# Optimization experiments

Measured on AMD Instinct MI355X. Metric: run time of the kernel, lower is better.

## Reference

```python
import jax, jax.numpy as jnp
import numpy as np

NMS_THRESH = 0.5
SCORE_THRESH = 0.2
MAX_SUBJECT = 15
MAX_OBJECT = 15
B, NS, NO = 32, 512, 512


def _make_boxes(k, b, n):
    u = jax.random.uniform(k, (b, n, 4))
    xy = u[..., :2] * 1000.0          # top-left corner
    wh = u[..., 2:] * 200.0 + 1.0     # positive width/height
    return jnp.concatenate([xy, xy + wh], axis=-1)  # valid xyxy boxes


def setup_inputs() -> dict:
    key = jax.random.key(0)
    ks = jax.random.split(key, 6)
    return {
        "subj_boxes": _make_boxes(ks[0], B, NS),
        "subj_scores": jax.random.uniform(ks[1], (B, NS)),
        "subj_labels": jax.random.randint(ks[2], (B, NS), 0, 30, dtype=jnp.int32),
        "obj_boxes": _make_boxes(ks[3], B, NO),
        "obj_scores": jax.random.uniform(ks[4], (B, NO)),
        "obj_labels": jax.random.randint(ks[5], (B, NO), 0, 30, dtype=jnp.int32),
    }


def reference(subj_boxes, subj_scores, subj_labels, obj_boxes, obj_scores, obj_labels):
    # concat subject + object detections per image, as in preprocess()
    boxes = jnp.concatenate([subj_boxes, obj_boxes], axis=1)    # [B,N,4]
    scores = jnp.concatenate([subj_scores, obj_scores], axis=1) # [B,N]
    labels = jnp.concatenate([subj_labels, obj_labels], axis=1) # [B,N]
    b, n = scores.shape
    is_subj = jnp.arange(n) < subj_boxes.shape[1]               # [N]

    # sort by score descending (matches the argsort after NMS; greedy NMS
    # preserves this ordering among survivors)
    order = jnp.argsort(-scores, axis=1)
    boxes = jnp.take_along_axis(boxes, order[..., None], axis=1)
    scores = jnp.take_along_axis(scores, order, axis=1)
    labels = jnp.take_along_axis(labels, order, axis=1)
    is_subj = jnp.take(is_subj, order)                          # [B,N]

    active = scores >= SCORE_THRESH

    # torchvision batched_nms: offset boxes per class so distinct classes
    # never overlap (comparisons only -> no gradient path)
    max_coord = jax.lax.stop_gradient(jnp.max(boxes))
    ob = boxes + labels.astype(boxes.dtype)[..., None] * (max_coord + 1.0)

    # pairwise IoU [B,N,N]
    area = (ob[..., 2] - ob[..., 0]) * (ob[..., 3] - ob[..., 1])
    lt = jnp.maximum(ob[:, :, None, :2], ob[:, None, :, :2])
    rb = jnp.minimum(ob[:, :, None, 2:], ob[:, None, :, 2:])
    wh = jnp.clip(rb - lt, 0.0)
    inter = wh[..., 0] * wh[..., 1]
    iou = inter / (area[:, :, None] + area[:, None, :] - inter)

    later = jnp.arange(n)[None, :] > jnp.arange(n)[:, None]     # strictly lower-score

    def body(i, suppressed):  # greedy NMS, vectorized over batch
        keep_i = active[:, i] & ~suppressed[:, i]
        return suppressed | (keep_i[:, None] & (iou[:, i, :] > NMS_THRESH) & later[i])

    suppressed = jax.lax.fori_loop(0, n, body, jnp.zeros((b, n), dtype=bool))
    kept = active & ~suppressed

    # split survivors into subjects / objects, keep top max_subject/max_object
    neg = jnp.finfo(scores.dtype).min
    sub_key = jnp.where(kept & is_subj, scores, neg)
    obj_key = jnp.where(kept & ~is_subj, scores, neg)
    sv, si = jax.lax.top_k(sub_key, MAX_SUBJECT)
    ov, oi = jax.lax.top_k(obj_key, MAX_OBJECT)
    idx = jnp.concatenate([si, oi], axis=1)                     # [B,K]
    valid = jnp.concatenate([sv, ov], axis=1) > neg             # [B,K]

    out_boxes = jnp.take_along_axis(boxes, idx[..., None], axis=1) * valid[..., None]
    out_scores = jnp.take_along_axis(scores, idx, axis=1) * valid
    out_labels = jnp.where(valid, jnp.take_along_axis(labels, idx, axis=1), -1)
    num_subjects = jnp.sum(sv > neg, axis=1)
    return out_boxes, out_scores, out_labels, num_subjects, valid
```

## Files before the change

### kernel.cpp

```cpp
#include <hip/hip_runtime.h>
#include <stdint.h>

#define BQ    32
#define NSUB  512
#define NDET  1024
#define NCLS  30
#define KSLOT 30
#define BCAP  96

#pragma clang fp contract(off)

typedef unsigned long long u64;

__global__ __launch_bounds__(512) void bucket_kernel(
    const float* __restrict__ sb, const float* __restrict__ ss,
    const int*   __restrict__ sl,
    const float* __restrict__ ob, const float* __restrict__ os,
    const int*   __restrict__ ol,
    float* __restrict__ pmax, int* __restrict__ cnts,
    u64* __restrict__ bkeys, float4* __restrict__ bboxes)
{
    const int b = blockIdx.x, t = threadIdx.x;
    const int lane = t & 63, w = t >> 6;
    __shared__ int   lcnt[NCLS];
    __shared__ float wred[8];

    if (t < NCLS) lcnt[t] = 0;

    float4 bxs = *(const float4*)(sb + (size_t)(b * NSUB + t) * 4);
    float4 bxo = *(const float4*)(ob + (size_t)(b * NSUB + t) * 4);
    float scs = ss[b * NSUB + t];  int lbs = sl[b * NSUB + t];
    float sco = os[b * NSUB + t];  int lbo = ol[b * NSUB + t];

    float m = fmaxf(fmaxf(fmaxf(bxs.x, bxs.y), fmaxf(bxs.z, bxs.w)),
                    fmaxf(fmaxf(bxo.x, bxo.y), fmaxf(bxo.z, bxo.w)));
    for (int off = 32; off; off >>= 1) m = fmaxf(m, __shfl_xor(m, off));
    if (lane == 0) wred[w] = m;
    __syncthreads();
    if (t == 0) {
        float mm = wred[0];
        for (int i = 1; i < 8; ++i) mm = fmaxf(mm, wred[i]);
        pmax[b] = mm;
    }

    if (scs >= 0.2f) {
        int pos = atomicAdd(&lcnt[lbs], 1);
        if (pos < BCAP) {
            size_t s = ((size_t)b * NCLS + lbs) * BCAP + pos;
            bkeys[s]  = ((u64)__float_as_uint(scs) << 32) | (u64)(1023 - t);
            bboxes[s] = bxs;
        }
    }
    if (sco >= 0.2f) {
        int pos = atomicAdd(&lcnt[lbo], 1);
        if (pos < BCAP) {
            size_t s = ((size_t)b * NCLS + lbo) * BCAP + pos;
            bkeys[s]  = ((u64)__float_as_uint(sco) << 32) | (u64)(1023 - (512 + t));
            bboxes[s] = bxo;
        }
    }
    __syncthreads();
    if (t < NCLS) {
        int c = lcnt[t];
        cnts[b * NCLS + t] = (c < BCAP) ? c : BCAP;
    }
}

__global__ __launch_bounds__(64) void nms_class_kernel(
    const float* __restrict__ pmax, const int* __restrict__ cnts,
    const u64* __restrict__ bkeys, const float4* __restrict__ bboxes,
    u64* __restrict__ subk, u64* __restrict__ objk)
{
#pragma clang fp contract(off)
    const int c    = blockIdx.x;
    const int b    = blockIdx.y;
    const int lane = threadIdx.x;

    __shared__ u64    keyarr[BCAP];
    __shared__ u64    skey[BCAP];
    __shared__ float4 bxs4[BCAP];

    const size_t base = (size_t)b * NCLS + c;

    u64    K1 = bkeys[base * BCAP + lane];
    float4 B1 = bboxes[base * BCAP + lane];
    u64 K2 = 0; float4 B2 = make_float4(0.f, 0.f, 0.f, 0.f);
    if (lane < BCAP - 64) {
        K2 = bkeys[base * BCAP + 64 + lane];
        B2 = bboxes[base * BCAP + 64 + lane];
    }
    const int cnt = cnts[base];
    float pv = pmax[lane & 31];
    for (int off = 32; off; off >>= 1) pv = fmaxf(pv, __shfl_xor(pv, off));
    const float mco  = pv + 1.0f;
    const float offc = (float)c * mco;

    keyarr[lane] = K1;
    if (lane < BCAP - 64) keyarr[64 + lane] = K2;
    __threadfence_block();

    {
        int r = 0;
        for (int l = 0; l < cnt; ++l) r += (keyarr[l] > K1) ? 1 : 0;
        if (lane < cnt) { skey[r] = K1; bxs4[r] = B1; }
    }
    if (cnt > 64) {
        int e = 64 + lane;
        int r = 0;
        for (int l = 0; l < cnt; ++l) r += (keyarr[l] > K2) ? 1 : 0;
        if (e < cnt) { skey[r] = K2; bxs4[r] = B2; }
    }
    __threadfence_block();

    const int  lim1  = (cnt < 64) ? cnt : 64;
    const bool have1 = (lane < lim1);
    u64 SK1 = have1 ? skey[lane] : 0;
    int idx1 = 1023 - (int)(unsigned)(SK1 & 0xffffffffull);
    float4 bj1 = have1 ? bxs4[lane] : make_float4(0.f, 0.f, 0.f, 0.f);
    const bool have2 = (64 + lane) < cnt;
    u64 SK2 = 0; int idx2 = 0; float4 bj2 = make_float4(0.f, 0.f, 0.f, 0.f);
    if (cnt > 64) {
        SK2 = have2 ? skey[64 + lane] : 0;
        idx2 = 1023 - (int)(unsigned)(SK2 & 0xffffffffull);
        if (have2) bj2 = bxs4[64 + lane];
    }

    float j0 = bj1.x + offc, j1 = bj1.y + offc;
    float j2v = bj1.z + offc, j3 = bj1.w + offc;
    float aj = (j2v - j0) * (j3 - j1);
    u64 ov = 0;
    for (int l = 0; l < lim1; ++l) {
        float4 bl = bxs4[l];
        float i0 = bl.x + offc, i1 = bl.y + offc;
        float i2 = bl.z + offc, i3 = bl.w + offc;
        float ai = (i2 - i0) * (i3 - i1);
        if (have1 && l < lane) {
            float ltx = fmaxf(i0, j0), lty = fmaxf(i1, j1);
            float rbx = fminf(i2, j2v), rby = fminf(i3, j3);
            float wx = fmaxf(rbx - ltx, 0.0f), wy = fmaxf(rby - lty, 0.0f);
            float inter = wx * wy;
            float iou = inter / ((ai + aj) - inter);
            if (iou > 0.5f) ov |= (1ull << l);
        }
    }
    bool sup1 = !have1;
    for (int l = 0; l < lim1; ++l) {
        u64 bal = __ballot(sup1);
        if (!((bal >> l) & 1ull)) sup1 = sup1 || (((ov >> l) & 1ull) != 0ull);
    }
    const bool kept1 = have1 && !sup1;
    const u64 keptA = __ballot(kept1);

    bool kept2 = false;
    if (cnt > 64) {
        float k0 = bj2.x + offc, k1 = bj2.y + offc;
        float k2 = bj2.z + offc, k3 = bj2.w + offc;
        float ak = (k2 - k0) * (k3 - k1);
        bool sup2 = !have2;
        for (int l = 0; l < 64; ++l) {
            if ((keptA >> l) & 1ull) {
                float4 bl = bxs4[l];
                float i0 = bl.x + offc, i1 = bl.y + offc;
                float i2 = bl.z + offc, i3 = bl.w + offc;
                float ai = (i2 - i0) * (i3 - i1);
                if (!sup2) {
                    float ltx = fmaxf(i0, k0), lty = fmaxf(i1, k1);
                    float rbx = fminf(i2, k2), rby = fminf(i3, k3);
                    float wx = fmaxf(rbx - ltx, 0.0f), wy = fmaxf(rby - lty, 0.0f);
                    float inter = wx * wy;
                    float iou = inter / ((ai + ak) - inter);
                    if (iou > 0.5f) sup2 = true;
                }
            }
        }
        u64 ov2 = 0;
        const int lim2 = cnt - 64;
        for (int l = 0; l < lim2; ++l) {
            float4 bl = bxs4[64 + l];
            float i0 = bl.x + offc, i1 = bl.y + offc;
            float i2 = bl.z + offc, i3 = bl.w + offc;
            float ai = (i2 - i0) * (i3 - i1);
            if (have2 && l < lane) {
                float ltx = fmaxf(i0, k0), lty = fmaxf(i1, k1);
                float rbx = fminf(i2, k2), rby = fminf(i3, k3);
                float wx = fmaxf(rbx - ltx, 0.0f), wy = fmaxf(rby - lty, 0.0f);
                float inter = wx * wy;
                float iou = inter / ((ai + ak) - inter);
                if (iou > 0.5f) ov2 |= (1ull << l);
            }
        }
        for (int l = 0; l < lim2; ++l) {
            u64 bal = __ballot(sup2);
            if (!((bal >> l) & 1ull)) sup2 = sup2 || (((ov2 >> l) & 1ull) != 0ull);
        }
        kept2 = have2 && !sup2;
    }

    const bool s1 = kept1 && (idx1 < NSUB), o1 = kept1 && (idx1 >= NSUB);
    const bool s2 = kept2 && (idx2 < NSUB), o2 = kept2 && (idx2 >= NSUB);
    const u64 mS1 = __ballot(s1), mS2 = __ballot(s2);
    const u64 mO1 = __ballot(o1), mO2 = __ballot(o2);
    const u64 ltm = (1ull << lane) - 1ull;
    u64* subp = subk + base * 15;
    u64* objp = objk + base * 15;
    if (s1) { int p = (int)__popcll(mS1 & ltm); if (p < 15) subp[p] = SK1; }
    if (s2) { int p = (int)__popcll(mS1) + (int)__popcll(mS2 & ltm); if (p < 15) subp[p] = SK2; }
    if (o1) { int p = (int)__popcll(mO1 & ltm); if (p < 15) objp[p] = SK1; }
    if (o2) { int p = (int)__popcll(mO1) + (int)__popcll(mO2 & ltm); if (p < 15) objp[p] = SK2; }
    int tS = (int)(__popcll(mS1) + __popcll(mS2)); if (tS > 15) tS = 15;
    int tO = (int)(__popcll(mO1) + __popcll(mO2)); if (tO > 15) tO = 15;
    if (lane >= tS && lane < 15) subp[lane] = 0;
    if (lane >= tO && lane < 15) objp[lane] = 0;
}

__global__ __launch_bounds__(64) void select_kernel(
    const float* __restrict__ sb, const int* __restrict__ sl,
    const float* __restrict__ ob, const int* __restrict__ ol,
    const u64* __restrict__ subk, const u64* __restrict__ objk,
    float* __restrict__ out)
{
    const int b    = blockIdx.x;
    const int side = blockIdx.y;
    const int lane = threadIdx.x;

    float* outB = out;
    float* outS = out + BQ * KSLOT * 4;
    float* outL = outS + BQ * KSLOT;
    float* outN = outL + BQ * KSLOT;
    float* outV = outN + BQ;

    const u64* src = (side ? objk : subk) + (size_t)b * NCLS * 15;
    u64 kk[8];
    #pragma unroll
    for (int i = 0; i < 8; ++i) {
        int p = lane + 64 * i;
        kk[i] = (p < NCLS * 15) ? src[p] : 0;
    }
    int nvalid = 0;
    for (int r = 0; r < 15; ++r) {
        u64 lm = 0; int li = 0;
        #pragma unroll
        for (int i = 0; i < 8; ++i) if (kk[i] > lm) { lm = kk[i]; li = i; }
        u64 gm = lm;
        for (int off = 32; off; off >>= 1) {
            u64 o = __shfl_xor(gm, off);
            if (o > gm) gm = o;
        }
        int p = b * KSLOT + (side ? (15 + r) : r);
        if (gm == 0) {
            if (lane == 0) {
                *(float4*)(outB + (size_t)p * 4) = make_float4(0.f, 0.f, 0.f, 0.f);
                outS[p] = 0.0f; outL[p] = -1.0f; outV[p] = 0.0f;
            }
        } else {
            u64 win = __ballot(lm == gm);
            int wl = (int)__ffsll(win) - 1;
            if (lane == wl) {
                kk[li] = 0;
                int idx = 1023 - (int)(unsigned)(gm & 0xffffffffull);
                float score = __uint_as_float((unsigned)(gm >> 32));
                float4 bx; int lb;
                if (idx < NSUB) {
                    bx = *(const float4*)(sb + (size_t)(b * NSUB + idx) * 4);
                    lb = sl[b * NSUB + idx];
                } else {
                    bx = *(const float4*)(ob + (size_t)(b * NSUB + idx - NSUB) * 4);
                    lb = ol[b * NSUB + idx - NSUB];
                }
                *(float4*)(outB + (size_t)p * 4) = bx;
                outS[p] = score;
                outL[p] = (float)lb;
                outV[p] = 1.0f;
            }
            nvalid++;
        }
    }
    if (side == 0 && lane == 0) outN[b] = (float)nvalid;
}

extern "C" void kernel_launch(void* const* d_in, const int* in_sizes, int n_in,
                              void* d_out, int out_size, void* d_ws, size_t ws_size,
                              hipStream_t stream) {
    const float* sb = (const float*)d_in[0];
    const float* ss = (const float*)d_in[1];
    const int*   sl = (const int*)d_in[2];
    const float* ob = (const float*)d_in[3];
    const float* os = (const float*)d_in[4];
    const int*   ol = (const int*)d_in[5];

    float*  pmax   = (float*)d_ws;
    int*    cnts   = (int*)((char*)d_ws + 256);
    u64*    bkeys  = (u64*)((char*)d_ws + 8192);
    float4* bboxes = (float4*)((char*)d_ws + 745472);
    u64*    subk   = (u64*)((char*)d_ws + 2220032);
    u64*    objk   = subk + (size_t)BQ * NCLS * 15;

    bucket_kernel<<<dim3(BQ), dim3(512), 0, stream>>>(
        sb, ss, sl, ob, os, ol, pmax, cnts, bkeys, bboxes);
    nms_class_kernel<<<dim3(NCLS, BQ), dim3(64), 0, stream>>>(
        pmax, cnts, bkeys, bboxes, subk, objk);
    select_kernel<<<dim3(BQ, 2), dim3(64), 0, stream>>>(
        sb, sl, ob, ol, subk, objk, (float*)d_out);
}
```

Measured before the change: 88.54 us.

## Fuse bucketing, per-class NMS and top-k selection into one per-image kernel

```diff
diff --git a/kernel.cpp b/kernel.cpp
--- a/kernel.cpp
+++ b/kernel.cpp
@@ -7,275 +7,259 @@
 #define NCLS  30
 #define KSLOT 30
 #define BCAP  96
+#define NTHR  1024
+#define NWAVE 16
 
 #pragma clang fp contract(off)
 
 typedef unsigned long long u64;
 
-__global__ __launch_bounds__(512) void bucket_kernel(
+__global__ __launch_bounds__(NTHR, 1) void fused_nms_kernel(
     const float* __restrict__ sb, const float* __restrict__ ss,
     const int*   __restrict__ sl,
     const float* __restrict__ ob, const float* __restrict__ os,
     const int*   __restrict__ ol,
-    float* __restrict__ pmax, int* __restrict__ cnts,
-    u64* __restrict__ bkeys, float4* __restrict__ bboxes)
+    float* __restrict__ out)
 {
+#pragma clang fp contract(off)
     const int b = blockIdx.x, t = threadIdx.x;
     const int lane = t & 63, w = t >> 6;
-    __shared__ int   lcnt[NCLS];
-    __shared__ float wred[8];
-
-    if (t < NCLS) lcnt[t] = 0;
-
-    float4 bxs = *(const float4*)(sb + (size_t)(b * NSUB + t) * 4);
-    float4 bxo = *(const float4*)(ob + (size_t)(b * NSUB + t) * 4);
-    float scs = ss[b * NSUB + t];  int lbs = sl[b * NSUB + t];
-    float sco = os[b * NSUB + t];  int lbo = ol[b * NSUB + t];
-
-    float m = fmaxf(fmaxf(fmaxf(bxs.x, bxs.y), fmaxf(bxs.z, bxs.w)),
-                    fmaxf(fmaxf(bxo.x, bxo.y), fmaxf(bxo.z, bxo.w)));
+
+    __shared__ u64    bkey[NCLS][BCAP];
+    __shared__ float4 bbox[NCLS][BCAP];
+    __shared__ u64    skey[NWAVE][BCAP];
+    __shared__ float4 sbox[NWAVE][BCAP];
+    __shared__ u64    outk[2][NCLS * 15];
+    __shared__ float4 outbx[2][NCLS * 15];
+    __shared__ int    lcnt[NCLS];
+    __shared__ float  wred[NWAVE];
+    __shared__ float  gmaxs;
+
+    const float4* sb4 = (const float4*)sb;
+    const float4* ob4 = (const float4*)ob;
+
+    float m = -__builtin_inff();
+    for (int i = t; i < BQ * NSUB; i += NTHR) {
+        float4 a = sb4[i], c4 = ob4[i];
+        m = fmaxf(m, fmaxf(fmaxf(a.x, a.y), fmaxf(a.z, a.w)));
+        m = fmaxf(m, fmaxf(fmaxf(c4.x, c4.y), fmaxf(c4.z, c4.w)));
+    }
     for (int off = 32; off; off >>= 1) m = fmaxf(m, __shfl_xor(m, off));
     if (lane == 0) wred[w] = m;
+    if (t < NCLS) lcnt[t] = 0;
     __syncthreads();
     if (t == 0) {
         float mm = wred[0];
-        for (int i = 1; i < 8; ++i) mm = fmaxf(mm, wred[i]);
-        pmax[b] = mm;
-    }
-
-    if (scs >= 0.2f) {
-        int pos = atomicAdd(&lcnt[lbs], 1);
-        if (pos < BCAP) {
-            size_t s = ((size_t)b * NCLS + lbs) * BCAP + pos;
-            bkeys[s]  = ((u64)__float_as_uint(scs) << 32) | (u64)(1023 - t);
-            bboxes[s] = bxs;
-        }
-    }
-    if (sco >= 0.2f) {
-        int pos = atomicAdd(&lcnt[lbo], 1);
-        if (pos < BCAP) {
-            size_t s = ((size_t)b * NCLS + lbo) * BCAP + pos;
-            bkeys[s]  = ((u64)__float_as_uint(sco) << 32) | (u64)(1023 - (512 + t));
-            bboxes[s] = bxo;
+        for (int i = 1; i < NWAVE; ++i) mm = fmaxf(mm, wred[i]);
+        gmaxs = mm;
+    }
+
+    {
+        float4 bx; float sc; int lb;
+        if (t < NSUB) {
+            bx = sb4[b * NSUB + t];
+            sc = ss[b * NSUB + t];
+            lb = sl[b * NSUB + t];
+        } else {
+            int j = t - NSUB;
+            bx = ob4[b * NSUB + j];
+            sc = os[b * NSUB + j];
+            lb = ol[b * NSUB + j];
+        }
+        if (sc >= 0.2f) {
+            int pos = atomicAdd(&lcnt[lb], 1);
+            if (pos < BCAP) {
+                bkey[lb][pos] = ((u64)__float_as_uint(sc) << 32) | (u64)(1023 - t);
+                bbox[lb][pos] = bx;
+            }
         }
     }
     __syncthreads();
-    if (t < NCLS) {
-        int c = lcnt[t];
-        cnts[b * NCLS + t] = (c < BCAP) ? c : BCAP;
-    }
-}
-
-__global__ __launch_bounds__(64) void nms_class_kernel(
-    const float* __restrict__ pmax, const int* __restrict__ cnts,
-    const u64* __restrict__ bkeys, const float4* __restrict__ bboxes,
-    u64* __restrict__ subk, u64* __restrict__ objk)
-{
-#pragma clang fp contract(off)
-    const int c    = blockIdx.x;
-    const int b    = blockIdx.y;
-    const int lane = threadIdx.x;
-
-    __shared__ u64    keyarr[BCAP];
-    __shared__ u64    skey[BCAP];
-    __shared__ float4 bxs4[BCAP];
-
-    const size_t base = (size_t)b * NCLS + c;
-
-    u64    K1 = bkeys[base * BCAP + lane];
-    float4 B1 = bboxes[base * BCAP + lane];
-    u64 K2 = 0; float4 B2 = make_float4(0.f, 0.f, 0.f, 0.f);
-    if (lane < BCAP - 64) {
-        K2 = bkeys[base * BCAP + 64 + lane];
-        B2 = bboxes[base * BCAP + 64 + lane];
-    }
-    const int cnt = cnts[base];
-    float pv = pmax[lane & 31];
-    for (int off = 32; off; off >>= 1) pv = fmaxf(pv, __shfl_xor(pv, off));
-    const float mco  = pv + 1.0f;
-    const float offc = (float)c * mco;
-
-    keyarr[lane] = K1;
-    if (lane < BCAP - 64) keyarr[64 + lane] = K2;
-    __threadfence_block();
-
-    {
-        int r = 0;
-        for (int l = 0; l < cnt; ++l) r += (keyarr[l] > K1) ? 1 : 0;
-        if (lane < cnt) { skey[r] = K1; bxs4[r] = B1; }
-    }
-    if (cnt > 64) {
-        int e = 64 + lane;
-        int r = 0;
-        for (int l = 0; l < cnt; ++l) r += (keyarr[l] > K2) ? 1 : 0;
-        if (e < cnt) { skey[r] = K2; bxs4[r] = B2; }
-    }
-    __threadfence_block();
-
-    const int  lim1  = (cnt < 64) ? cnt : 64;
-    const bool have1 = (lane < lim1);
-    u64 SK1 = have1 ? skey[lane] : 0;
-    int idx1 = 1023 - (int)(unsigned)(SK1 & 0xffffffffull);
-    float4 bj1 = have1 ? bxs4[lane] : make_float4(0.f, 0.f, 0.f, 0.f);
-    const bool have2 = (64 + lane) < cnt;
-    u64 SK2 = 0; int idx2 = 0; float4 bj2 = make_float4(0.f, 0.f, 0.f, 0.f);
-    if (cnt > 64) {
-        SK2 = have2 ? skey[64 + lane] : 0;
-        idx2 = 1023 - (int)(unsigned)(SK2 & 0xffffffffull);
-        if (have2) bj2 = bxs4[64 + lane];
-    }
-
-    float j0 = bj1.x + offc, j1 = bj1.y + offc;
-    float j2v = bj1.z + offc, j3 = bj1.w + offc;
-    float aj = (j2v - j0) * (j3 - j1);
-    u64 ov = 0;
-    for (int l = 0; l < lim1; ++l) {
-        float4 bl = bxs4[l];
-        float i0 = bl.x + offc, i1 = bl.y + offc;
-        float i2 = bl.z + offc, i3 = bl.w + offc;
-        float ai = (i2 - i0) * (i3 - i1);
-        if (have1 && l < lane) {
-            float ltx = fmaxf(i0, j0), lty = fmaxf(i1, j1);
-            float rbx = fminf(i2, j2v), rby = fminf(i3, j3);
-            float wx = fmaxf(rbx - ltx, 0.0f), wy = fmaxf(rby - lty, 0.0f);
-            float inter = wx * wy;
-            float iou = inter / ((ai + aj) - inter);
-            if (iou > 0.5f) ov |= (1ull << l);
-        }
-    }
-    bool sup1 = !have1;
-    for (int l = 0; l < lim1; ++l) {
-        u64 bal = __ballot(sup1);
-        if (!((bal >> l) & 1ull)) sup1 = sup1 || (((ov >> l) & 1ull) != 0ull);
-    }
-    const bool kept1 = have1 && !sup1;
-    const u64 keptA = __ballot(kept1);
-
-    bool kept2 = false;
-    if (cnt > 64) {
-        float k0 = bj2.x + offc, k1 = bj2.y + offc;
-        float k2 = bj2.z + offc, k3 = bj2.w + offc;
-        float ak = (k2 - k0) * (k3 - k1);
-        bool sup2 = !have2;
-        for (int l = 0; l < 64; ++l) {
-            if ((keptA >> l) & 1ull) {
-                float4 bl = bxs4[l];
+    const float mco = gmaxs + 1.0f;
+
+    for (int rr = 0; rr < 2; ++rr) {
+        const int c = w + NWAVE * rr;
+        if (c >= NCLS) break;
+        int cnt = lcnt[c]; if (cnt > BCAP) cnt = BCAP;
+        const float offc = (float)c * mco;
+
+        u64    K1 = bkey[c][lane];
+        float4 B1 = bbox[c][lane];
+        u64 K2 = 0; float4 B2 = make_float4(0.f, 0.f, 0.f, 0.f);
+        if (lane < BCAP - 64) {
+            K2 = bkey[c][64 + lane];
+            B2 = bbox[c][64 + lane];
+        }
+
+        {
+            int r = 0;
+            for (int l = 0; l < cnt; ++l) r += (bkey[c][l] > K1) ? 1 : 0;
+            if (lane < cnt) { skey[w][r] = K1; sbox[w][r] = B1; }
+        }
+        if (cnt > 64) {
+            int e = 64 + lane;
+            int r = 0;
+            for (int l = 0; l < cnt; ++l) r += (bkey[c][l] > K2) ? 1 : 0;
+            if (e < cnt) { skey[w][r] = K2; sbox[w][r] = B2; }
+        }
+        __threadfence_block();
+
+        const int  lim1  = (cnt < 64) ? cnt : 64;
+        const bool have1 = (lane < lim1);
+        u64 SK1 = have1 ? skey[w][lane] : 0;
+        int idx1 = 1023 - (int)(unsigned)(SK1 & 0xffffffffull);
+        float4 bj1 = have1 ? sbox[w][lane] : make_float4(0.f, 0.f, 0.f, 0.f);
+        const bool have2 = (64 + lane) < cnt;
+        u64 SK2 = 0; int idx2 = 0; float4 bj2 = make_float4(0.f, 0.f, 0.f, 0.f);
+        if (cnt > 64) {
+            SK2 = have2 ? skey[w][64 + lane] : 0;
+            idx2 = 1023 - (int)(unsigned)(SK2 & 0xffffffffull);
+            if (have2) bj2 = sbox[w][64 + lane];
+        }
+
+        float j0 = bj1.x + offc, j1 = bj1.y + offc;
+        float j2v = bj1.z + offc, j3 = bj1.w + offc;
+        float aj = (j2v - j0) * (j3 - j1);
+        u64 ov = 0;
+        for (int l = 0; l < lim1; ++l) {
+            float4 bl = sbox[w][l];
+            float i0 = bl.x + offc, i1 = bl.y + offc;
+            float i2 = bl.z + offc, i3 = bl.w + offc;
+            float ai = (i2 - i0) * (i3 - i1);
+            if (have1 && l < lane) {
+                float ltx = fmaxf(i0, j0), lty = fmaxf(i1, j1);
+                float rbx = fminf(i2, j2v), rby = fminf(i3, j3);
+                float wx = fmaxf(rbx - ltx, 0.0f), wy = fmaxf(rby - lty, 0.0f);
+                float inter = wx * wy;
+                float iou = inter / ((ai + aj) - inter);
+                if (iou > 0.5f) ov |= (1ull << l);
+            }
+        }
+        bool sup1 = !have1;
+        for (int l = 0; l < lim1; ++l) {
+            u64 bal = __ballot(sup1);
+            if (!((bal >> l) & 1ull)) sup1 = sup1 || (((ov >> l) & 1ull) != 0ull);
+        }
+        const bool kept1 = have1 && !sup1;
+        const u64 keptA = __ballot(kept1);
+
+        bool kept2 = false;
+        if (cnt > 64) {
+            float k0 = bj2.x + offc, k1 = bj2.y + offc;
+            float k2 = bj2.z + offc, k3 = bj2.w + offc;
+            float ak = (k2 - k0) * (k3 - k1);
+            bool sup2 = !have2;
+            for (int l = 0; l < 64; ++l) {
+                if ((keptA >> l) & 1ull) {
+                    float4 bl = sbox[w][l];
+                    float i0 = bl.x + offc, i1 = bl.y + offc;
+                    float i2 = bl.z + offc, i3 = bl.w + offc;
+                    float ai = (i2 - i0) * (i3 - i1);
+                    if (!sup2) {
+                        float ltx = fmaxf(i0, k0), lty = fmaxf(i1, k1);
+                        float rbx = fminf(i2, k2), rby = fminf(i3, k3);
+                        float wx = fmaxf(rbx - ltx, 0.0f), wy = fmaxf(rby - lty, 0.0f);
+                        float inter = wx * wy;
+                        float iou = inter / ((ai + ak) - inter);
+                        if (iou > 0.5f) sup2 = true;
+                    }
+                }
+            }
+            u64 ov2 = 0;
+            const int lim2 = cnt - 64;
+            for (int l = 0; l < lim2; ++l) {
+                float4 bl = sbox[w][64 + l];
                 float i0 = bl.x + offc, i1 = bl.y + offc;
                 float i2 = bl.z + offc, i3 = bl.w + offc;
                 float ai = (i2 - i0) * (i3 - i1);
-                if (!sup2) {
+                if (have2 && l < lane) {
                     float ltx = fmaxf(i0, k0), lty = fmaxf(i1, k1);
                     float rbx = fminf(i2, k2), rby = fminf(i3, k3);
                     float wx = fmaxf(rbx - ltx, 0.0f), wy = fmaxf(rby - lty, 0.0f);
                     float inter = wx * wy;
                     float iou = inter / ((ai + ak) - inter);
-                    if (iou > 0.5f) sup2 = true;
-                }
-            }
-        }
-        u64 ov2 = 0;
-        const int lim2 = cnt - 64;
-        for (int l = 0; l < lim2; ++l) {
-            float4 bl = bxs4[64 + l];
-            float i0 = bl.x + offc, i1 = bl.y + offc;
-            float i2 = bl.z + offc, i3 = bl.w + offc;
-            float ai = (i2 - i0) * (i3 - i1);
-            if (have2 && l < lane) {
-                float ltx = fmaxf(i0, k0), lty = fmaxf(i1, k1);
-                float rbx = fminf(i2, k2), rby = fminf(i3, k3);
-                float wx = fmaxf(rbx - ltx, 0.0f), wy = fmaxf(rby - lty, 0.0f);
-                float inter = wx * wy;
-                float iou = inter / ((ai + ak) - inter);
-                if (iou > 0.5f) ov2 |= (1ull << l);
-            }
-        }
-        for (int l = 0; l < lim2; ++l) {
-            u64 bal = __ballot(sup2);
-            if (!((bal >> l) & 1ull)) sup2 = sup2 || (((ov2 >> l) & 1ull) != 0ull);
-        }
-        kept2 = have2 && !sup2;
-    }
-
-    const bool s1 = kept1 && (idx1 < NSUB), o1 = kept1 && (idx1 >= NSUB);
-    const bool s2 = kept2 && (idx2 < NSUB), o2 = kept2 && (idx2 >= NSUB);
-    const u64 mS1 = __ballot(s1), mS2 = __ballot(s2);
-    const u64 mO1 = __ballot(o1), mO2 = __ballot(o2);
-    const u64 ltm = (1ull << lane) - 1ull;
-    u64* subp = subk + base * 15;
-    u64* objp = objk + base * 15;
-    if (s1) { int p = (int)__popcll(mS1 & ltm); if (p < 15) subp[p] = SK1; }
-    if (s2) { int p = (int)__popcll(mS1) + (int)__popcll(mS2 & ltm); if (p < 15) subp[p] = SK2; }
-    if (o1) { int p = (int)__popcll(mO1 & ltm); if (p < 15) objp[p] = SK1; }
-    if (o2) { int p = (int)__popcll(mO1) + (int)__popcll(mO2 & ltm); if (p < 15) objp[p] = SK2; }
-    int tS = (int)(__popcll(mS1) + __popcll(mS2)); if (tS > 15) tS = 15;
-    int tO = (int)(__popcll(mO1) + __popcll(mO2)); if (tO > 15) tO = 15;
-    if (lane >= tS && lane < 15) subp[lane] = 0;
-    if (lane >= tO && lane < 15) objp[lane] = 0;
-}
-
-__global__ __launch_bounds__(64) void select_kernel(
-    const float* __restrict__ sb, const int* __restrict__ sl,
-    const float* __restrict__ ob, const int* __restrict__ ol,
-    const u64* __restrict__ subk, const u64* __restrict__ objk,
-    float* __restrict__ out)
-{
-    const int b    = blockIdx.x;
-    const int side = blockIdx.y;
-    const int lane = threadIdx.x;
-
-    float* outB = out;
-    float* outS = out + BQ * KSLOT * 4;
-    float* outL = outS + BQ * KSLOT;
-    float* outN = outL + BQ * KSLOT;
-    float* outV = outN + BQ;
-
-    const u64* src = (side ? objk : subk) + (size_t)b * NCLS * 15;
-    u64 kk[8];
-    #pragma unroll
-    for (int i = 0; i < 8; ++i) {
-        int p = lane + 64 * i;
-        kk[i] = (p < NCLS * 15) ? src[p] : 0;
-    }
-    int nvalid = 0;
-    for (int r = 0; r < 15; ++r) {
-        u64 lm = 0; int li = 0;
+                    if (iou > 0.5f) ov2 |= (1ull << l);
+                }
+            }
+            for (int l = 0; l < lim2; ++l) {
+                u64 bal = __ballot(sup2);
+                if (!((bal >> l) & 1ull)) sup2 = sup2 || (((ov2 >> l) & 1ull) != 0ull);
+            }
+            kept2 = have2 && !sup2;
+        }
+
+        const bool s1 = kept1 && (idx1 < NSUB), o1 = kept1 && (idx1 >= NSUB);
+        const bool s2 = kept2 && (idx2 < NSUB), o2 = kept2 && (idx2 >= NSUB);
+        const u64 mS1 = __ballot(s1), mS2 = __ballot(s2);
+        const u64 mO1 = __ballot(o1), mO2 = __ballot(o2);
+        const u64 ltm = (1ull << lane) - 1ull;
+        u64*    skp = &outk[0][c * 15];  float4* sbp = &outbx[0][c * 15];
+        u64*    okp = &outk[1][c * 15];  float4* obp = &outbx[1][c * 15];
+        if (s1) { int p = (int)__popcll(mS1 & ltm); if (p < 15) { skp[p] = SK1; sbp[p] = bj1; } }
+        if (s2) { int p = (int)__popcll(mS1) + (int)__popcll(mS2 & ltm); if (p < 15) { skp[p] = SK2; sbp[p] = bj2; } }
+        if (o1) { int p = (int)__popcll(mO1 & ltm); if (p < 15) { okp[p] = SK1; obp[p] = bj1; } }
+        if (o2) { int p = (int)__popcll(mO1) + (int)__popcll(mO2 & ltm); if (p < 15) { okp[p] = SK2; obp[p] = bj2; } }
+        int tS = (int)(__popcll(mS1) + __popcll(mS2)); if (tS > 15) tS = 15;
+        int tO = (int)(__popcll(mO1) + __popcll(mO2)); if (tO > 15) tO = 15;
+        if (lane >= tS && lane < 15) skp[lane] = 0;
+        if (lane >= tO && lane < 15) okp[lane] = 0;
+    }
+    __syncthreads();
+
+    if (w < 2) {
+        const int side = w;
+        float* outB = out;
+        float* outS = out + BQ * KSLOT * 4;
+        float* outL = outS + BQ * KSLOT;
+        float* outN = outL + BQ * KSLOT;
+        float* outV = outN + BQ;
+
+        const u64*    src  = outk[side];
+        const float4* srcb = outbx[side];
+        u64 kk[8];
         #pragma unroll
-        for (int i = 0; i < 8; ++i) if (kk[i] > lm) { lm = kk[i]; li = i; }
-        u64 gm = lm;
-        for (int off = 32; off; off >>= 1) {
-            u64 o = __shfl_xor(gm, off);
-            if (o > gm) gm = o;
-        }
-        int p = b * KSLOT + (side ? (15 + r) : r);
-        if (gm == 0) {
-            if (lane == 0) {
-                *(float4*)(outB + (size_t)p * 4) = make_float4(0.f, 0.f, 0.f, 0.f);
-                outS[p] = 0.0f; outL[p] = -1.0f; outV[p] = 0.0f;
-            }
-        } else {
-            u64 win = __ballot(lm == gm);
-            int wl = (int)__ffsll(win) - 1;
-            if (lane == wl) {
-                kk[li] = 0;
-                int idx = 1023 - (int)(unsigned)(gm & 0xffffffffull);
-                float score = __uint_as_float((unsigned)(gm >> 32));
-                float4 bx; int lb;
-                if (idx < NSUB) {
-                    bx = *(const float4*)(sb + (size_t)(b * NSUB + idx) * 4);
-                    lb = sl[b * NSUB + idx];
-                } else {
-                    bx = *(const float4*)(ob + (size_t)(b * NSUB + idx - NSUB) * 4);
-                    lb = ol[b * NSUB + idx - NSUB];
-                }
-                *(float4*)(outB + (size_t)p * 4) = bx;
-                outS[p] = score;
-                outL[p] = (float)lb;
-                outV[p] = 1.0f;
-            }
-            nvalid++;
-        }
-    }
-    if (side == 0 && lane == 0) outN[b] = (float)nvalid;
+        for (int i = 0; i < 8; ++i) {
+            int p = lane + 64 * i;
+            kk[i] = (p < NCLS * 15) ? src[p] : 0;
+        }
+        int nvalid = 0;
+        for (int r = 0; r < 15; ++r) {
+            u64 lm = 0;
+            #pragma unroll
+            for (int i = 0; i < 8; ++i) lm = (kk[i] > lm) ? kk[i] : lm;
+            u64 gm = lm;
+            for (int off = 32; off; off >>= 1) {
+                u64 o = __shfl_xor(gm, off);
+                if (o > gm) gm = o;
+            }
+            int p = b * KSLOT + (side ? (15 + r) : r);
+            if (gm == 0) {
+                if (lane == 0) {
+                    *(float4*)(outB + (size_t)p * 4) = make_float4(0.f, 0.f, 0.f, 0.f);
+                    outS[p] = 0.0f; outL[p] = -1.0f; outV[p] = 0.0f;
+                }
+            } else {
+                u64 win = __ballot(lm == gm);
+                int wl = (int)__ffsll(win) - 1;
+                if (lane == wl) {
+                    int sp = 0;
+                    #pragma unroll
+                    for (int i = 0; i < 8; ++i) if (kk[i] == gm) sp = lane + 64 * i;
+                    #pragma unroll
+                    for (int i = 0; i < 8; ++i) if (kk[i] == gm) kk[i] = 0;
+                    float4 bx = srcb[sp];
+                    float score = __uint_as_float((unsigned)(gm >> 32));
+                    int cls = sp / 15;
+                    *(float4*)(outB + (size_t)p * 4) = bx;
+                    outS[p] = score;
+                    outL[p] = (float)cls;
+                    outV[p] = 1.0f;
+                }
+                nvalid++;
+            }
+        }
+        if (side == 0 && lane == 0) outN[b] = (float)nvalid;
+    }
 }
 
 extern "C" void kernel_launch(void* const* d_in, const int* in_sizes, int n_in,
@@ -288,17 +272,6 @@
     const float* os = (const float*)d_in[4];
     const int*   ol = (const int*)d_in[5];
 
-    float*  pmax   = (float*)d_ws;
-    int*    cnts   = (int*)((char*)d_ws + 256);
-    u64*    bkeys  = (u64*)((char*)d_ws + 8192);
-    float4* bboxes = (float4*)((char*)d_ws + 745472);
-    u64*    subk   = (u64*)((char*)d_ws + 2220032);
-    u64*    objk   = subk + (size_t)BQ * NCLS * 15;
-
-    bucket_kernel<<<dim3(BQ), dim3(512), 0, stream>>>(
-        sb, ss, sl, ob, os, ol, pmax, cnts, bkeys, bboxes);
-    nms_class_kernel<<<dim3(NCLS, BQ), dim3(64), 0, stream>>>(
-        pmax, cnts, bkeys, bboxes, subk, objk);
-    select_kernel<<<dim3(BQ, 2), dim3(64), 0, stream>>>(
-        sb, sl, ob, ol, subk, objk, (float*)d_out);
+    fused_nms_kernel<<<dim3(BQ), dim3(NTHR), 0, stream>>>(
+        sb, ss, sl, ob, os, ol, (float*)d_out);
 }
```

Result: slower. 104.7 us (+18.2%).
